# Optimization experiments

Hardware: AMD Instinct MI355X
Metric: run time of the kernel (lower is better)

Reference implementation:

```python
import jax, jax.numpy as jnp
import numpy as np

N = 1_000_000
D = 128            # node feature dim
G = 25_000         # number of graphs (num_segments, static)
STEPS = 8


def setup_inputs() -> dict:
    key = jax.random.key(0)
    k1, k2, k3 = jax.random.split(key, 3)
    node_feature = jax.random.normal(k1, (N, D), dtype=jnp.float32)
    graph_indicator = jnp.sort(jax.random.randint(k2, (N,), 0, G, dtype=jnp.int32))
    # glorot-ish small init for recurrent kernel (carry_dim=2D -> 4*D gates)
    recurrent_kernel = jax.random.normal(k3, (2 * D, 4 * D), dtype=jnp.float32) * 0.05
    bias = jnp.zeros((4 * D,), dtype=jnp.float32)
    return {
        "node_feature": node_feature,
        "graph_indicator": graph_indicator,
        "recurrent_kernel": recurrent_kernel,
        "bias": bias,
    }


def _segment_softmax(score, seg_ids, num_segments):
    # numerically-stable per-segment softmax over a flat score vector [N]
    smax = jax.ops.segment_max(score, seg_ids, num_segments=num_segments)
    e = jnp.exp(score - smax[seg_ids])
    denom = jax.ops.segment_sum(e, seg_ids, num_segments=num_segments)
    return e / denom[seg_ids]


def reference(node_feature, graph_indicator, recurrent_kernel, bias):
    d = node_feature.shape[-1]
    memory_state = jnp.zeros((G, d), dtype=node_feature.dtype)
    carry_state = jnp.zeros((G, d), dtype=node_feature.dtype)
    carry_state_evolved = None
    for _ in range(STEPS):
        # attention score per node: <node_feature, carry of its graph>
        carry_exp = carry_state[graph_indicator]                  # [N, d]
        score = jnp.sum(node_feature * carry_exp, axis=1)         # [N]
        attn = _segment_softmax(score, graph_indicator, G)        # [N]
        readout = jax.ops.segment_sum(attn[:, None] * node_feature,
                                      graph_indicator, num_segments=G)  # [G, d]
        carry_state_evolved = jnp.concatenate([carry_state, readout], axis=1)  # [G, 2d]
        # NoInputLSTMCell
        z = carry_state_evolved @ recurrent_kernel + bias          # [G, 4d]
        u, f, c, o = jnp.split(z, 4, axis=1)
        memory_state = jax.nn.sigmoid(f) * memory_state + jax.nn.sigmoid(u) * jnp.tanh(c)
        carry_state = jax.nn.sigmoid(o) * jnp.tanh(memory_state)
    return carry_state_evolved
```

## Files before the change

kernel.cpp:

```cpp
#include <hip/hip_runtime.h>
#include <stdint.h>

#define DD  128
#define G2D 256
#define G4D 512

typedef float  f32x4  __attribute__((ext_vector_type(4)));
typedef short  s16x8  __attribute__((ext_vector_type(8)));
typedef __bf16 bf16x8 __attribute__((ext_vector_type(8)));

__device__ __forceinline__ short f2bf(float f) {
  unsigned u = __builtin_bit_cast(unsigned, f);
  u += 0x7FFFu + ((u >> 16) & 1u);
  return (short)(u >> 16);
}
__device__ __forceinline__ float bf2f(short s) {
  unsigned u = ((unsigned)(unsigned short)s) << 16;
  return __builtin_bit_cast(float, u);
}
__device__ __forceinline__ float sigmoidf_(float x) {
  return 1.f / (1.f + __expf(-x));
}
__device__ __forceinline__ float tanhf_(float x) {
  x = fminf(fmaxf(x, -15.f), 15.f);
  float e = __expf(2.f * x);
  return (e - 1.f) / (e + 1.f);
}

__global__ void seg_kernel(const int* __restrict__ ind, int* __restrict__ seg,
                           int N, int G) {
  int g = blockIdx.x * blockDim.x + threadIdx.x;
  if (g > G) return;
  int lo = 0, hi = N;
  while (lo < hi) {
    int mid = (lo + hi) >> 1;
    if (ind[mid] < g) lo = mid + 1; else hi = mid;
  }
  seg[g] = lo;
}

__global__ void nfconv_kernel(const float* __restrict__ nf,
                              short* __restrict__ nfb) {
  size_t idx = (size_t)blockIdx.x * blockDim.x + threadIdx.x;
  const f32x4* src = (const f32x4*)nf + idx * 2;
  f32x4 a = src[0], b = src[1];
  s16x8 o;
  o[0] = f2bf(a.x); o[1] = f2bf(a.y); o[2] = f2bf(a.z); o[3] = f2bf(a.w);
  o[4] = f2bf(b.x); o[5] = f2bf(b.y); o[6] = f2bf(b.z); o[7] = f2bf(b.w);
  ((s16x8*)nfb)[idx] = o;
}

__global__ void wconv_kernel(const float* __restrict__ W, short* __restrict__ WT) {
  int idx = blockIdx.x * blockDim.x + threadIdx.x;
  int n = idx & (G4D - 1);
  int k = idx >> 9;
  WT[(size_t)n * G2D + k] = f2bf(W[(size_t)k * G4D + n]);
}

__global__ void __launch_bounds__(256) passa_kernel(
    const short* __restrict__ nfb, float* __restrict__ ce,
    const int* __restrict__ seg, int G) {
  int wid = (blockIdx.x * blockDim.x + threadIdx.x) >> 6;
  if (wid >= G) return;
  int lane = threadIdx.x & 63;
  int gq = lane >> 4;
  int sl = lane & 15;
  int s0 = seg[wid], s1 = seg[wid + 1];
  int n  = s1 - s0;
  float* cerow = ce + (size_t)wid * G2D;
  if (n == 0) {
    if (gq == 0) {
      f32x4 z = {0.f, 0.f, 0.f, 0.f};
      *(f32x4*)(cerow + DD + sl * 8)     = z;
      *(f32x4*)(cerow + DD + sl * 8 + 4) = z;
    }
    return;
  }
  f32x4 c0 = *(const f32x4*)(cerow + sl * 8);
  f32x4 c1 = *(const f32x4*)(cerow + sl * 8 + 4);
  float m = -1e30f, l = 0.f;
  float acc[8];
  #pragma unroll
  for (int k = 0; k < 8; k++) acc[k] = 0.f;
  const short* base = nfb + (size_t)s0 * DD + sl * 8;

  auto body = [&](int j) {
    s16x8 xr = *(const s16x8*)(base + (size_t)j * DD);
    float xf[8];
    #pragma unroll
    for (int k = 0; k < 8; k++) xf[k] = bf2f(xr[k]);
    float s = xf[0]*c0.x + xf[1]*c0.y + xf[2]*c0.z + xf[3]*c0.w
            + xf[4]*c1.x + xf[5]*c1.y + xf[6]*c1.z + xf[7]*c1.w;
    #pragma unroll
    for (int off = 1; off < 16; off <<= 1) s += __shfl_xor(s, off, 64);
    float nm = fmaxf(m, s);
    float sc = __expf(m - nm);
    float p  = __expf(s - nm);
    l = l * sc + p;
    #pragma unroll
    for (int k = 0; k < 8; k++) acc[k] = acc[k] * sc + p * xf[k];
    m = nm;
  };

  int nfull = n >> 2;
  #pragma unroll 2
  for (int i = 0; i < nfull; i++) body(i * 4 + gq);
  int rem = n & 3;
  if (gq < rem) body(nfull * 4 + gq);

  #pragma unroll
  for (int w = 16; w <= 32; w <<= 1) {
    float m2 = __shfl_xor(m, w, 64);
    float l2 = __shfl_xor(l, w, 64);
    float M  = fmaxf(m, m2);
    float e1 = __expf(m - M);
    float e2 = __expf(m2 - M);
    l = l * e1 + l2 * e2;
    #pragma unroll
    for (int k = 0; k < 8; k++) {
      float a2 = __shfl_xor(acc[k], w, 64);
      acc[k] = acc[k] * e1 + a2 * e2;
    }
    m = M;
  }
  if (gq == 0) {
    float inv = 1.f / l;
    f32x4 r0, r1;
    r0.x = acc[0]*inv; r0.y = acc[1]*inv; r0.z = acc[2]*inv; r0.w = acc[3]*inv;
    r1.x = acc[4]*inv; r1.y = acc[5]*inv; r1.z = acc[6]*inv; r1.w = acc[7]*inv;
    *(f32x4*)(cerow + DD + sl * 8)     = r0;
    *(f32x4*)(cerow + DD + sl * 8 + 4) = r1;
  }
}

__global__ void __launch_bounds__(256) lstm_kernel(
    float* __restrict__ ce, const short* __restrict__ WT,
    const float* __restrict__ bias, float* __restrict__ mem, int G) {
  __shared__ __align__(16) short As[16][264];
  int m0 = blockIdx.x * 16;
  int t  = threadIdx.x;
  #pragma unroll
  for (int rep = 0; rep < 4; rep++) {
    int idx = rep * 256 + t;
    int row = idx >> 6;
    int cv  = idx & 63;
    int g   = m0 + row;
    f32x4 v = {0.f, 0.f, 0.f, 0.f};
    if (g < G) v = *(const f32x4*)(ce + (size_t)g * G2D + cv * 4);
    As[row][cv * 4 + 0] = f2bf(v.x);
    As[row][cv * 4 + 1] = f2bf(v.y);
    As[row][cv * 4 + 2] = f2bf(v.z);
    As[row][cv * 4 + 3] = f2bf(v.w);
  }
  __syncthreads();
  int wid  = t >> 6;
  int lane = t & 63;
  int quad = lane >> 4;
  int l16  = lane & 15;
  int cb   = wid * 32;
  f32x4 zero4 = {0.f, 0.f, 0.f, 0.f};
  f32x4 acc[4][2];
  #pragma unroll
  for (int gi = 0; gi < 4; gi++)
    #pragma unroll
    for (int ns = 0; ns < 2; ns++) acc[gi][ns] = zero4;
  #pragma unroll
  for (int kc = 0; kc < 8; kc++) {
    int k0 = kc * 32 + quad * 8;
    s16x8 a = *(const s16x8*)(&As[l16][k0]);
    #pragma unroll
    for (int gi = 0; gi < 4; gi++) {
      #pragma unroll
      for (int ns = 0; ns < 2; ns++) {
        int ncol = gi * DD + cb + ns * 16 + l16;
        s16x8 b = *(const s16x8*)(WT + (size_t)ncol * G2D + k0);
        acc[gi][ns] = __builtin_amdgcn_mfma_f32_16x16x32_bf16(
            __builtin_bit_cast(bf16x8, a), __builtin_bit_cast(bf16x8, b),
            acc[gi][ns], 0, 0, 0);
      }
    }
  }
  #pragma unroll
  for (int ns = 0; ns < 2; ns++) {
    int col = cb + ns * 16 + l16;
    float bu = bias[0 * DD + col];
    float bf = bias[1 * DD + col];
    float bc = bias[2 * DD + col];
    float bo = bias[3 * DD + col];
    #pragma unroll
    for (int r = 0; r < 4; r++) {
      int g = m0 + quad * 4 + r;
      if (g < G) {
        float u = acc[0][ns][r] + bu;
        float f = acc[1][ns][r] + bf;
        float c = acc[2][ns][r] + bc;
        float o = acc[3][ns][r] + bo;
        float mo = mem[(size_t)g * DD + col];
        float mn = sigmoidf_(f) * mo + sigmoidf_(u) * tanhf_(c);
        mem[(size_t)g * DD + col] = mn;
        ce[(size_t)g * G2D + col] = sigmoidf_(o) * tanhf_(mn);
      }
    }
  }
}

extern "C" void kernel_launch(void* const* d_in, const int* in_sizes, int n_in,
                              void* d_out, int out_size, void* d_ws, size_t ws_size,
                              hipStream_t stream) {
  const float* nf   = (const float*)d_in[0];
  const int*   ind  = (const int*)d_in[1];
  const float* W    = (const float*)d_in[2];
  const float* bias = (const float*)d_in[3];
  int N = in_sizes[1];
  int G = out_size / G2D;

  char* ws = (char*)d_ws;
  size_t off = 0;
  float* ce  = (float*)(ws + off); off += (size_t)G * G2D * 4;
  float* mem = (float*)(ws + off); off += (size_t)G * DD * 4;
  short* WT  = (short*)(ws + off); off += (size_t)G2D * G4D * 2;
  int*   seg = (int*)(ws + off);   off += (size_t)(G + 1) * 4;
  off = (off + 255) & ~(size_t)255;
  short* nfb = (short*)(ws + off); off += (size_t)N * DD * 2;
  (void)ws_size; (void)n_in;

  nfconv_kernel<<<(int)(((size_t)N * DD / 8 + 255) / 256), 256, 0, stream>>>(nf, nfb);
  hipMemsetAsync(ce, 0, (size_t)G * G2D * 4 + (size_t)G * DD * 4, stream);
  seg_kernel<<<(G + 256) / 256, 256, 0, stream>>>(ind, seg, N, G);
  wconv_kernel<<<(G2D * G4D) / 256, 256, 0, stream>>>(W, WT);

  int pa_blocks   = (G + 3) / 4;
  int lstm_blocks = (G + 15) / 16;
  for (int step = 0; step < 8; step++) {
    passa_kernel<<<pa_blocks, 256, 0, stream>>>(nfb, ce, seg, G);
    if (step < 7)
      lstm_kernel<<<lstm_blocks, 256, 0, stream>>>(ce, WT, bias, mem, G);
  }
  hipMemcpyAsync(d_out, ce, (size_t)out_size * 4, hipMemcpyDeviceToDevice, stream);
}
```

Measured before the change: 1.586 ms.

## Fuse all attention and LSTM steps into one persistent per-graph-block kernel

Replaces the per-step attention and LSTM kernel launches with a single kernel. Each block owns 8 graphs, caches up to 64 of each graph's node rows as bf16 in LDS, keeps LSTM weights in registers, and holds carry and memory state in shared memory across all 8 steps. Step 0 takes a plain mean, since the carry is zero there. This removes the global bf16 conversion pass, the repeated global reads of node features, and the round trips of carry state through global memory. In exchange, occupancy drops because of heavy LDS and register use, and rows beyond 64 per graph are re-read from global memory in fp32 every step.

New measurement: 1.319 ms. 16.8% less time.

```diff
diff --git a/kernel.cpp b/kernel.cpp
--- a/kernel.cpp
+++ b/kernel.cpp
@@ -1,11 +1,15 @@
 #include <hip/hip_runtime.h>
 #include <stdint.h>
 
-#define DD  128
-#define G2D 256
-#define G4D 512
+#define DD   128
+#define G2D  256
+#define G4D  512
+#define GPB  8
+#define SLOT 64
+#define ASTR 264
 
 typedef float  f32x4  __attribute__((ext_vector_type(4)));
+typedef short  s16x4  __attribute__((ext_vector_type(4)));
 typedef short  s16x8  __attribute__((ext_vector_type(8)));
 typedef __bf16 bf16x8 __attribute__((ext_vector_type(8)));
 
@@ -39,17 +43,6 @@
   seg[g] = lo;
 }
 
-__global__ void nfconv_kernel(const float* __restrict__ nf,
-                              short* __restrict__ nfb) {
-  size_t idx = (size_t)blockIdx.x * blockDim.x + threadIdx.x;
-  const f32x4* src = (const f32x4*)nf + idx * 2;
-  f32x4 a = src[0], b = src[1];
-  s16x8 o;
-  o[0] = f2bf(a.x); o[1] = f2bf(a.y); o[2] = f2bf(a.z); o[3] = f2bf(a.w);
-  o[4] = f2bf(b.x); o[5] = f2bf(b.y); o[6] = f2bf(b.z); o[7] = f2bf(b.w);
-  ((s16x8*)nfb)[idx] = o;
-}
-
 __global__ void wconv_kernel(const float* __restrict__ W, short* __restrict__ WT) {
   int idx = blockIdx.x * blockDim.x + threadIdx.x;
   int n = idx & (G4D - 1);
@@ -57,150 +50,221 @@
   WT[(size_t)n * G2D + k] = f2bf(W[(size_t)k * G4D + n]);
 }
 
-__global__ void __launch_bounds__(256) passa_kernel(
-    const short* __restrict__ nfb, float* __restrict__ ce,
-    const int* __restrict__ seg, int G) {
-  int wid = (blockIdx.x * blockDim.x + threadIdx.x) >> 6;
-  if (wid >= G) return;
-  int lane = threadIdx.x & 63;
-  int gq = lane >> 4;
-  int sl = lane & 15;
-  int s0 = seg[wid], s1 = seg[wid + 1];
-  int n  = s1 - s0;
-  float* cerow = ce + (size_t)wid * G2D;
-  if (n == 0) {
-    if (gq == 0) {
-      f32x4 z = {0.f, 0.f, 0.f, 0.f};
-      *(f32x4*)(cerow + DD + sl * 8)     = z;
-      *(f32x4*)(cerow + DD + sl * 8 + 4) = z;
-    }
-    return;
-  }
-  f32x4 c0 = *(const f32x4*)(cerow + sl * 8);
-  f32x4 c1 = *(const f32x4*)(cerow + sl * 8 + 4);
-  float m = -1e30f, l = 0.f;
-  float acc[8];
+__global__ void __launch_bounds__(512) fused_kernel(
+    const float* __restrict__ nf, const int* __restrict__ seg,
+    const short* __restrict__ WT, const float* __restrict__ bias,
+    float* __restrict__ out, int G) {
+  extern __shared__ char smem[];
+  short* nfb   = (short*)smem;
+  short* A     = (short*)(smem + GPB * SLOT * DD * 2);
+  float* carry = (float*)(smem + GPB * SLOT * DD * 2 + 16 * ASTR * 2);
+  float* mem   = (float*)((char*)carry + GPB * DD * 4);
+
+  const int t    = threadIdx.x;
+  const int w    = t >> 6;
+  const int lane = t & 63;
+  const int gq   = lane >> 4;
+  const int sl   = lane & 15;
+  const int g0   = blockIdx.x * GPB;
+  const int g    = g0 + w;
+  const bool active = (g < G);
+
+  {
+    int* az = (int*)A;
+    for (int i = t; i < (16 * ASTR) / 2; i += 512) az[i] = 0;
+    for (int i = t; i < GPB * DD; i += 512) mem[i] = 0.f;
+  }
+  int s0 = 0, n = 0;
+  if (active) { s0 = seg[g]; n = seg[g + 1] - s0; }
+  carry[w * DD + lane]      = 0.f;
+  carry[w * DD + 64 + lane] = 0.f;
+  __syncthreads();
+
+  short* slot = nfb + w * (SLOT * DD);
+  const int nl = n < SLOT ? n : SLOT;
+  {
+    const int r2 = lane >> 5;
+    const int c  = lane & 31;
+    const int iters = (nl + 1) >> 1;
+    f32x4 vc; int rowc = r2; bool okc = rowc < nl;
+    if (okc) vc = *((const f32x4*)(nf + (size_t)(s0 + rowc) * DD) + c);
+    for (int i = 0; i < iters; ++i) {
+      const int rown = (i + 1) * 2 + r2;
+      f32x4 vn; const bool okn = rown < nl;
+      if (okn) vn = *((const f32x4*)(nf + (size_t)(s0 + rown) * DD) + c);
+      if (okc) {
+        s16x4 o;
+        o[0] = f2bf(vc.x); o[1] = f2bf(vc.y); o[2] = f2bf(vc.z); o[3] = f2bf(vc.w);
+        *(s16x4*)(slot + (size_t)rowc * DD + c * 4) = o;
+      }
+      vc = vn; rowc = rown; okc = okn;
+    }
+  }
+
+  s16x8 bw[8][4];
   #pragma unroll
-  for (int k = 0; k < 8; k++) acc[k] = 0.f;
-  const short* base = nfb + (size_t)s0 * DD + sl * 8;
-
-  auto body = [&](int j) {
-    s16x8 xr = *(const s16x8*)(base + (size_t)j * DD);
-    float xf[8];
+  for (int kc = 0; kc < 8; ++kc) {
+    const int k0 = kc * 32 + gq * 8;
     #pragma unroll
-    for (int k = 0; k < 8; k++) xf[k] = bf2f(xr[k]);
-    float s = xf[0]*c0.x + xf[1]*c0.y + xf[2]*c0.z + xf[3]*c0.w
-            + xf[4]*c1.x + xf[5]*c1.y + xf[6]*c1.z + xf[7]*c1.w;
+    for (int gi = 0; gi < 4; ++gi) {
+      const int ncol = gi * DD + w * 16 + sl;
+      bw[kc][gi] = *(const s16x8*)(WT + (size_t)ncol * G2D + k0);
+    }
+  }
+  const int colB = w * 16 + sl;
+  const float bU = bias[0 * DD + colB], bF = bias[1 * DD + colB],
+              bC = bias[2 * DD + colB], bO = bias[3 * DD + colB];
+
+  #pragma unroll 1
+  for (int step = 0; step < 8; ++step) {
+    float r[8];
     #pragma unroll
-    for (int off = 1; off < 16; off <<= 1) s += __shfl_xor(s, off, 64);
-    float nm = fmaxf(m, s);
-    float sc = __expf(m - nm);
-    float p  = __expf(s - nm);
-    l = l * sc + p;
+    for (int k = 0; k < 8; ++k) r[k] = 0.f;
+
+    if (active && n > 0) {
+      float m = -1e30f, l = 0.f;
+      float acc[8];
+      #pragma unroll
+      for (int k = 0; k < 8; ++k) acc[k] = 0.f;
+
+      if (step == 0) {
+        const int nfull = nl >> 2, rem = nl & 3;
+        #pragma unroll 2
+        for (int i = 0; i < nfull; ++i) {
+          s16x8 xr = *(const s16x8*)(slot + (size_t)(i * 4 + gq) * DD + sl * 8);
+          #pragma unroll
+          for (int k = 0; k < 8; ++k) acc[k] += bf2f(xr[k]);
+          l += 1.f;
+        }
+        if (gq < rem) {
+          s16x8 xr = *(const s16x8*)(slot + (size_t)(nfull * 4 + gq) * DD + sl * 8);
+          #pragma unroll
+          for (int k = 0; k < 8; ++k) acc[k] += bf2f(xr[k]);
+          l += 1.f;
+        }
+        for (int j = SLOT + gq; j < n; j += 4) {
+          const f32x4* gp = (const f32x4*)(nf + (size_t)(s0 + j) * DD) + sl * 2;
+          const f32x4 a = gp[0], b = gp[1];
+          const float xf[8] = {a.x, a.y, a.z, a.w, b.x, b.y, b.z, b.w};
+          #pragma unroll
+          for (int k = 0; k < 8; ++k) acc[k] += xf[k];
+          l += 1.f;
+        }
+        m = 0.f;
+      } else {
+        const f32x4 c0 = *(const f32x4*)(carry + w * DD + sl * 8);
+        const f32x4 c1 = *(const f32x4*)(carry + w * DD + sl * 8 + 4);
+        auto upd = [&](const float xf[8]) {
+          float s = xf[0] * c0.x + xf[1] * c0.y + xf[2] * c0.z + xf[3] * c0.w
+                  + xf[4] * c1.x + xf[5] * c1.y + xf[6] * c1.z + xf[7] * c1.w;
+          #pragma unroll
+          for (int off = 1; off < 16; off <<= 1) s += __shfl_xor(s, off, 64);
+          const float nm = fmaxf(m, s);
+          const float sc = __expf(m - nm);
+          const float p  = __expf(s - nm);
+          l = l * sc + p;
+          #pragma unroll
+          for (int k = 0; k < 8; ++k) acc[k] = acc[k] * sc + p * xf[k];
+          m = nm;
+        };
+        const int nfull = nl >> 2, rem = nl & 3;
+        #pragma unroll 2
+        for (int i = 0; i < nfull; ++i) {
+          s16x8 xr = *(const s16x8*)(slot + (size_t)(i * 4 + gq) * DD + sl * 8);
+          float xf[8];
+          #pragma unroll
+          for (int k = 0; k < 8; ++k) xf[k] = bf2f(xr[k]);
+          upd(xf);
+        }
+        if (gq < rem) {
+          s16x8 xr = *(const s16x8*)(slot + (size_t)(nfull * 4 + gq) * DD + sl * 8);
+          float xf[8];
+          #pragma unroll
+          for (int k = 0; k < 8; ++k) xf[k] = bf2f(xr[k]);
+          upd(xf);
+        }
+        for (int j = SLOT + gq; j < n; j += 4) {
+          const f32x4* gp = (const f32x4*)(nf + (size_t)(s0 + j) * DD) + sl * 2;
+          const f32x4 a = gp[0], b = gp[1];
+          const float xf[8] = {a.x, a.y, a.z, a.w, b.x, b.y, b.z, b.w};
+          upd(xf);
+        }
+      }
+      #pragma unroll
+      for (int ww = 16; ww <= 32; ww <<= 1) {
+        const float m2 = __shfl_xor(m, ww, 64);
+        const float l2 = __shfl_xor(l, ww, 64);
+        const float M  = fmaxf(m, m2);
+        const float e1 = __expf(m - M);
+        const float e2 = __expf(m2 - M);
+        l = l * e1 + l2 * e2;
+        #pragma unroll
+        for (int k = 0; k < 8; ++k) {
+          const float a2 = __shfl_xor(acc[k], ww, 64);
+          acc[k] = acc[k] * e1 + a2 * e2;
+        }
+        m = M;
+      }
+      if (gq == 0) {
+        const float inv = (l > 0.f) ? 1.f / l : 0.f;
+        s16x8 pk;
+        #pragma unroll
+        for (int k = 0; k < 8; ++k) { r[k] = acc[k] * inv; pk[k] = f2bf(r[k]); }
+        *(s16x8*)(A + w * ASTR + DD + sl * 8) = pk;
+      }
+    }
+
+    if (step == 7) {
+      if (active) {
+        if (gq == 0) {
+          f32x4 r0 = {r[0], r[1], r[2], r[3]};
+          f32x4 r1 = {r[4], r[5], r[6], r[7]};
+          *(f32x4*)(out + (size_t)g * G2D + DD + sl * 8)     = r0;
+          *(f32x4*)(out + (size_t)g * G2D + DD + sl * 8 + 4) = r1;
+        } else if (gq == 1) {
+          const f32x4 a = *(const f32x4*)(carry + w * DD + sl * 8);
+          const f32x4 b = *(const f32x4*)(carry + w * DD + sl * 8 + 4);
+          *(f32x4*)(out + (size_t)g * G2D + sl * 8)     = a;
+          *(f32x4*)(out + (size_t)g * G2D + sl * 8 + 4) = b;
+        }
+      }
+      break;
+    }
+    __syncthreads();
+
+    f32x4 az[4];
     #pragma unroll
-    for (int k = 0; k < 8; k++) acc[k] = acc[k] * sc + p * xf[k];
-    m = nm;
-  };
-
-  int nfull = n >> 2;
-  #pragma unroll 2
-  for (int i = 0; i < nfull; i++) body(i * 4 + gq);
-  int rem = n & 3;
-  if (gq < rem) body(nfull * 4 + gq);
-
-  #pragma unroll
-  for (int w = 16; w <= 32; w <<= 1) {
-    float m2 = __shfl_xor(m, w, 64);
-    float l2 = __shfl_xor(l, w, 64);
-    float M  = fmaxf(m, m2);
-    float e1 = __expf(m - M);
-    float e2 = __expf(m2 - M);
-    l = l * e1 + l2 * e2;
+    for (int gi = 0; gi < 4; ++gi) az[gi] = (f32x4){0.f, 0.f, 0.f, 0.f};
     #pragma unroll
-    for (int k = 0; k < 8; k++) {
-      float a2 = __shfl_xor(acc[k], w, 64);
-      acc[k] = acc[k] * e1 + a2 * e2;
-    }
-    m = M;
-  }
-  if (gq == 0) {
-    float inv = 1.f / l;
-    f32x4 r0, r1;
-    r0.x = acc[0]*inv; r0.y = acc[1]*inv; r0.z = acc[2]*inv; r0.w = acc[3]*inv;
-    r1.x = acc[4]*inv; r1.y = acc[5]*inv; r1.z = acc[6]*inv; r1.w = acc[7]*inv;
-    *(f32x4*)(cerow + DD + sl * 8)     = r0;
-    *(f32x4*)(cerow + DD + sl * 8 + 4) = r1;
-  }
-}
-
-__global__ void __launch_bounds__(256) lstm_kernel(
-    float* __restrict__ ce, const short* __restrict__ WT,
-    const float* __restrict__ bias, float* __restrict__ mem, int G) {
-  __shared__ __align__(16) short As[16][264];
-  int m0 = blockIdx.x * 16;
-  int t  = threadIdx.x;
-  #pragma unroll
-  for (int rep = 0; rep < 4; rep++) {
-    int idx = rep * 256 + t;
-    int row = idx >> 6;
-    int cv  = idx & 63;
-    int g   = m0 + row;
-    f32x4 v = {0.f, 0.f, 0.f, 0.f};
-    if (g < G) v = *(const f32x4*)(ce + (size_t)g * G2D + cv * 4);
-    As[row][cv * 4 + 0] = f2bf(v.x);
-    As[row][cv * 4 + 1] = f2bf(v.y);
-    As[row][cv * 4 + 2] = f2bf(v.z);
-    As[row][cv * 4 + 3] = f2bf(v.w);
-  }
-  __syncthreads();
-  int wid  = t >> 6;
-  int lane = t & 63;
-  int quad = lane >> 4;
-  int l16  = lane & 15;
-  int cb   = wid * 32;
-  f32x4 zero4 = {0.f, 0.f, 0.f, 0.f};
-  f32x4 acc[4][2];
-  #pragma unroll
-  for (int gi = 0; gi < 4; gi++)
-    #pragma unroll
-    for (int ns = 0; ns < 2; ns++) acc[gi][ns] = zero4;
-  #pragma unroll
-  for (int kc = 0; kc < 8; kc++) {
-    int k0 = kc * 32 + quad * 8;
-    s16x8 a = *(const s16x8*)(&As[l16][k0]);
-    #pragma unroll
-    for (int gi = 0; gi < 4; gi++) {
+    for (int kc = 0; kc < 8; ++kc) {
+      const int k0 = kc * 32 + gq * 8;
+      const s16x8 af = *(const s16x8*)(A + (size_t)sl * ASTR + k0);
       #pragma unroll
-      for (int ns = 0; ns < 2; ns++) {
-        int ncol = gi * DD + cb + ns * 16 + l16;
-        s16x8 b = *(const s16x8*)(WT + (size_t)ncol * G2D + k0);
-        acc[gi][ns] = __builtin_amdgcn_mfma_f32_16x16x32_bf16(
-            __builtin_bit_cast(bf16x8, a), __builtin_bit_cast(bf16x8, b),
-            acc[gi][ns], 0, 0, 0);
-      }
-    }
-  }
-  #pragma unroll
-  for (int ns = 0; ns < 2; ns++) {
-    int col = cb + ns * 16 + l16;
-    float bu = bias[0 * DD + col];
-    float bf = bias[1 * DD + col];
-    float bc = bias[2 * DD + col];
-    float bo = bias[3 * DD + col];
-    #pragma unroll
-    for (int r = 0; r < 4; r++) {
-      int g = m0 + quad * 4 + r;
-      if (g < G) {
-        float u = acc[0][ns][r] + bu;
-        float f = acc[1][ns][r] + bf;
-        float c = acc[2][ns][r] + bc;
-        float o = acc[3][ns][r] + bo;
-        float mo = mem[(size_t)g * DD + col];
-        float mn = sigmoidf_(f) * mo + sigmoidf_(u) * tanhf_(c);
-        mem[(size_t)g * DD + col] = mn;
-        ce[(size_t)g * G2D + col] = sigmoidf_(o) * tanhf_(mn);
-      }
-    }
+      for (int gi = 0; gi < 4; ++gi)
+        az[gi] = __builtin_amdgcn_mfma_f32_16x16x32_bf16(
+            __builtin_bit_cast(bf16x8, af), __builtin_bit_cast(bf16x8, bw[kc][gi]),
+            az[gi], 0, 0, 0);
+    }
+    __syncthreads();
+    if (gq < 2) {
+      #pragma unroll
+      for (int rr = 0; rr < 4; ++rr) {
+        const int gg = gq * 4 + rr;
+        if (g0 + gg < G) {
+          const float u = az[0][rr] + bU;
+          const float f = az[1][rr] + bF;
+          const float c = az[2][rr] + bC;
+          const float o = az[3][rr] + bO;
+          const float mo = mem[gg * DD + colB];
+          const float mn = sigmoidf_(f) * mo + sigmoidf_(u) * tanhf_(c);
+          mem[gg * DD + colB] = mn;
+          const float cn = sigmoidf_(o) * tanhf_(mn);
+          carry[gg * DD + colB] = cn;
+          A[gg * ASTR + colB] = f2bf(cn);
+        }
+      }
+    }
+    __syncthreads();
   }
 }
 
@@ -215,26 +279,23 @@
   int G = out_size / G2D;
 
   char* ws = (char*)d_ws;
-  size_t off = 0;
-  float* ce  = (float*)(ws + off); off += (size_t)G * G2D * 4;
-  float* mem = (float*)(ws + off); off += (size_t)G * DD * 4;
-  short* WT  = (short*)(ws + off); off += (size_t)G2D * G4D * 2;
-  int*   seg = (int*)(ws + off);   off += (size_t)(G + 1) * 4;
-  off = (off + 255) & ~(size_t)255;
-  short* nfb = (short*)(ws + off); off += (size_t)N * DD * 2;
+  short* WT  = (short*)ws;
+  int*   seg = (int*)(ws + 262144);
   (void)ws_size; (void)n_in;
 
-  nfconv_kernel<<<(int)(((size_t)N * DD / 8 + 255) / 256), 256, 0, stream>>>(nf, nfb);
-  hipMemsetAsync(ce, 0, (size_t)G * G2D * 4 + (size_t)G * DD * 4, stream);
   seg_kernel<<<(G + 256) / 256, 256, 0, stream>>>(ind, seg, N, G);
   wconv_kernel<<<(G2D * G4D) / 256, 256, 0, stream>>>(W, WT);
 
-  int pa_blocks   = (G + 3) / 4;
-  int lstm_blocks = (G + 15) / 16;
-  for (int step = 0; step < 8; step++) {
-    passa_kernel<<<pa_blocks, 256, 0, stream>>>(nfb, ce, seg, G);
-    if (step < 7)
-      lstm_kernel<<<lstm_blocks, 256, 0, stream>>>(ce, WT, bias, mem, G);
-  }
-  hipMemcpyAsync(d_out, ce, (size_t)out_size * 4, hipMemcpyDeviceToDevice, stream);
-}
+  const int SMEM_BYTES = GPB * SLOT * DD * 2
+                       + 16 * ASTR * 2
+                       + GPB * DD * 4
+                       + GPB * DD * 4;
+  static bool attr_set = false;
+  if (!attr_set) {
+    hipFuncSetAttribute(reinterpret_cast<const void*>(fused_kernel),
+                        hipFuncAttributeMaxDynamicSharedMemorySize, SMEM_BYTES);
+    attr_set = true;
+  }
+  fused_kernel<<<(G + GPB - 1) / GPB, 512, SMEM_BYTES, stream>>>(
+      nf, seg, WT, bias, (float*)d_out, G);
+}
```
